# Kernel tuning notes

Hardware: AMD Instinct MI355X
Metric: run time of the kernel (lower is better)

Reference implementation:

```python
import jax, jax.numpy as jnp
import numpy as np

N = 50000          # nodes
E = 800000         # edges
H, C = 8, 32       # heads, channels per head
HC = H * C         # 256
IN = 4             # input feature dim
SLOPE = 0.2        # LeakyReLU negative slope (PyG default)
EPS = 1e-16        # PyG softmax denominator eps


def gat_layer(x, src, dst, ea, W, a_s, a_d, W_e, a_e, b, add_self_loops):
    """Single PyG-style GATConv with edge_dim=1. x:[N,in], ea:[E,1]."""
    if add_self_loops:
        # fill_value='mean': self-loop edge_attr = mean of incoming edge_attr per node
        ones = jnp.ones((src.shape[0], 1), ea.dtype)
        cnt = jax.ops.segment_sum(ones, dst, num_segments=N)
        loop_ea = jax.ops.segment_sum(ea, dst, num_segments=N) / jnp.maximum(cnt, 1.0)
        loop = jnp.arange(N, dtype=src.dtype)
        src = jnp.concatenate([src, loop])
        dst = jnp.concatenate([dst, loop])
        ea = jnp.concatenate([ea, loop_ea], axis=0)
    h = (x @ W).reshape(-1, H, C)                       # [N,H,C] shared src/dst proj
    al_s = jnp.einsum('nhc,hc->nh', h, a_s)              # [N,H]
    al_d = jnp.einsum('nhc,hc->nh', h, a_d)              # [N,H]
    # lin_edge is [1 -> H*C] with no bias, so (lin_edge(ea) * att_edge).sum(-1)
    # collapses to ea * w_e with w_e[h] = sum_c W_e[h,c]*a_e[h,c]
    w_e = jnp.sum(W_e * a_e, axis=-1)                    # [H]
    logits = al_s[src] + al_d[dst] + ea * w_e[None, :]   # [E,H]
    logits = jax.nn.leaky_relu(logits, SLOPE)
    # segment softmax over destination node
    m = jax.ops.segment_max(logits, dst, num_segments=N)
    m = jnp.where(jnp.isfinite(m), m, 0.0)
    p = jnp.exp(logits - m[dst])
    denom = jax.ops.segment_sum(p, dst, num_segments=N)
    alpha = p / (denom[dst] + EPS)                       # [E,H]
    out = jax.ops.segment_sum(h[src] * alpha[:, :, None], dst, num_segments=N)
    return out.reshape(-1, HC) + b                       # concat heads + bias


def setup_inputs() -> dict:
    key = jax.random.key(0)
    ks = jax.random.split(key, 24)
    inp = {
        'x': jax.random.normal(ks[0], (N, IN), jnp.float32),
        'edge_index': jax.random.randint(ks[1], (2, E), 0, N, jnp.int32),
        'edge_attr': jax.random.uniform(ks[2], (E, 1), jnp.float32),
    }
    in_dims = [IN, HC, HC]
    ki = 3
    for l in range(3):
        d = in_dims[l]
        inp[f'W{l+1}'] = jax.random.normal(ks[ki], (d, HC), jnp.float32) * (1.0 / np.sqrt(d)); ki += 1
        inp[f'as{l+1}'] = jax.random.normal(ks[ki], (H, C), jnp.float32) * 0.1; ki += 1
        inp[f'ad{l+1}'] = jax.random.normal(ks[ki], (H, C), jnp.float32) * 0.1; ki += 1
        inp[f'We{l+1}'] = jax.random.normal(ks[ki], (H, C), jnp.float32) * 0.1; ki += 1
        inp[f'ae{l+1}'] = jax.random.normal(ks[ki], (H, C), jnp.float32) * 0.1; ki += 1
        inp[f'b{l+1}'] = jnp.zeros((HC,), jnp.float32)
    return inp


def reference(x, edge_index, edge_attr,
              W1, as1, ad1, We1, ae1, b1,
              W2, as2, ad2, We2, ae2, b2,
              W3, as3, ad3, We3, ae3, b3):
    src, dst = edge_index[0], edge_index[1]
    h = jax.nn.relu(gat_layer(x, src, dst, edge_attr, W1, as1, ad1, We1, ae1, b1, False))
    h = jax.nn.relu(gat_layer(h, src, dst, edge_attr, W2, as2, ad2, We2, ae2, b2, True))
    h = jax.nn.relu(gat_layer(h, src, dst, edge_attr, W3, as3, ad3, We3, ae3, b3, True))
    return h
```

## Files before the change

### kernel.cpp

```cpp
#include <hip/hip_runtime.h>
#include <hip/hip_fp16.h>
#include <math.h>

#define HEADS 8
#define HC 256
#define SLOPE 0.2f
#define SM_EPS 1e-16f
#define LDA 40

typedef __attribute__((ext_vector_type(4))) _Float16 half4v;
typedef __attribute__((ext_vector_type(8))) _Float16 half8;
typedef __attribute__((ext_vector_type(4))) float f32x4;

__global__ void hist_kernel(const int* __restrict__ dst, int* __restrict__ cnt,
                            int* __restrict__ rank, int E) {
  int e = blockIdx.x * blockDim.x + threadIdx.x;
  if (e < E) rank[e] = atomicAdd(&cnt[dst[e]], 1);
}

__global__ void scan_blocks(const int* __restrict__ cnt, int* __restrict__ excl,
                            int* __restrict__ bsums, int N) {
  __shared__ int wsum[16];
  int t = threadIdx.x;
  int i = blockIdx.x * 1024 + t;
  int v = (i < N) ? cnt[i] : 0;
  int lane = t & 63, w = t >> 6;
  int s = v;
  #pragma unroll
  for (int off = 1; off < 64; off <<= 1) {
    int u = __shfl_up(s, off);
    if (lane >= off) s += u;
  }
  if (lane == 63) wsum[w] = s;
  __syncthreads();
  if (w == 0) {
    int ws = (lane < 16) ? wsum[lane] : 0;
    #pragma unroll
    for (int off = 1; off < 16; off <<= 1) {
      int u = __shfl_up(ws, off);
      if (lane >= off) ws += u;
    }
    if (lane < 16) wsum[lane] = ws;
  }
  __syncthreads();
  int wo = (w == 0) ? 0 : wsum[w - 1];
  int incl = s + wo;
  if (i < N) excl[i] = incl - v;
  if (t == 1023) bsums[blockIdx.x] = incl;
}

__global__ void scan_sums(int* __restrict__ bsums, int nb) {
  int lane = threadIdx.x;
  int carry = 0;
  for (int c0 = 0; c0 < nb; c0 += 64) {
    int idx = c0 + lane;
    int v = (idx < nb) ? bsums[idx] : 0;
    int s = v;
    #pragma unroll
    for (int off = 1; off < 64; off <<= 1) {
      int u = __shfl_up(s, off);
      if (lane >= off) s += u;
    }
    if (idx < nb) bsums[idx] = carry + s - v;
    carry += __shfl(s, 63);
  }
}

__global__ void scan_apply(const int* __restrict__ bsums, int* __restrict__ row_ptr,
                           int N, int E) {
  int i = blockIdx.x * blockDim.x + threadIdx.x;
  if (i < N) row_ptr[i] += bsums[i >> 10];
  if (i == 0) row_ptr[N] = E;
}

__global__ void fill_kernel(const int* __restrict__ src, const int* __restrict__ dst,
                            const float* __restrict__ ea, const int* __restrict__ row_ptr,
                            const int* __restrict__ rank, int2* __restrict__ srcea, int E) {
  int e = blockIdx.x * blockDim.x + threadIdx.x;
  if (e < E) {
    int pos = row_ptr[dst[e]] + rank[e];
    srcea[pos] = make_int2(src[e], __float_as_int(ea[e]));
  }
}

__global__ void prep_kernel(const float* __restrict__ W2, __half* __restrict__ WT2,
                            const float* __restrict__ W3, __half* __restrict__ WT3,
                            const float* __restrict__ We1, const float* __restrict__ ae1,
                            const float* __restrict__ We2, const float* __restrict__ ae2,
                            const float* __restrict__ We3, const float* __restrict__ ae3,
                            float* __restrict__ wev,
                            const float* __restrict__ W1, const float* __restrict__ as1,
                            const float* __restrict__ ad1, float* __restrict__ vsd) {
  int b = blockIdx.x;
  int t = threadIdx.x;
  if (b < 256) {
    WT2[t * HC + b] = (__half)W2[b * HC + t];
  } else if (b < 512) {
    int k = b - 256;
    WT3[t * HC + k] = (__half)W3[k * HC + t];
  } else if (b < 515) {
    if (t >= 64) return;
    int l = b - 512;
    const float* We = (l == 0) ? We1 : (l == 1) ? We2 : We3;
    const float* ae = (l == 0) ? ae1 : (l == 1) ? ae2 : ae3;
    float p = 0.f;
    #pragma unroll
    for (int i = 0; i < 4; i++) p += We[t * 4 + i] * ae[t * 4 + i];
    p += __shfl_xor(p, 1);
    p += __shfl_xor(p, 2);
    p += __shfl_xor(p, 4);
    if ((t & 7) == 0) wev[l * 8 + (t >> 3)] = p;
  } else {
    if (t >= 64) return;
    int which = t >> 5;
    int idx = t & 31;
    int h = idx >> 2, k = idx & 3;
    const float* a = which ? ad1 : as1;
    float p = 0.f;
    #pragma unroll
    for (int c = 0; c < 32; c++) p += W1[k * HC + h * 32 + c] * a[h * 32 + c];
    vsd[which * 32 + idx] = p;
  }
}

__global__ __launch_bounds__(256) void mfma_gemm(
    const __half* __restrict__ A, const __half* __restrict__ WT,
    const float* __restrict__ a_s, const float* __restrict__ a_d,
    __half* __restrict__ Hh, float* __restrict__ als, float* __restrict__ ald, int M) {
  __shared__ _Float16 sA[64 * LDA], sB[128 * LDA];
  int t = threadIdx.x;
  int bm = blockIdx.x >> 1, bn = blockIdx.x & 1;
  int m0 = bm * 64, n0 = bn * 128;
  int wave = t >> 6, lane = t & 63, quad = lane >> 4, l16 = lane & 15;
  int sr = t >> 2;
  int sk = (t & 3) * 8;

  f32x4 acc[8];
  #pragma unroll
  for (int c = 0; c < 8; c++) acc[c] = (f32x4){0.f, 0.f, 0.f, 0.f};

  size_t ar = (size_t)min(m0 + sr, M - 1) * HC;
  size_t br0 = (size_t)(n0 + sr) * HC;
  size_t br1 = (size_t)(n0 + sr + 64) * HC;

  half8 pA = *(const half8*)(A + ar + sk);
  half8 pB0 = *(const half8*)(WT + br0 + sk);
  half8 pB1 = *(const half8*)(WT + br1 + sk);

  for (int k0 = 0; k0 < HC; k0 += 32) {
    __syncthreads();
    *(half8*)(sA + sr * LDA + sk) = pA;
    *(half8*)(sB + sr * LDA + sk) = pB0;
    *(half8*)(sB + (sr + 64) * LDA + sk) = pB1;
    __syncthreads();
    int kn = k0 + 32;
    if (kn < HC) {
      pA = *(const half8*)(A + ar + kn + sk);
      pB0 = *(const half8*)(WT + br0 + kn + sk);
      pB1 = *(const half8*)(WT + br1 + kn + sk);
    }
    half8 av = *(const half8*)(sA + (wave * 16 + l16) * LDA + quad * 8);
    #pragma unroll
    for (int c = 0; c < 8; c++) {
      half8 bv = *(const half8*)(sB + (c * 16 + l16) * LDA + quad * 8);
      acc[c] = __builtin_amdgcn_mfma_f32_16x16x32_f16(av, bv, acc[c], 0, 0, 0);
    }
  }

  float asv[8], adv[8];
  #pragma unroll
  for (int c = 0; c < 8; c++) {
    int col = n0 + c * 16 + l16;
    asv[c] = a_s[col];
    adv[c] = a_d[col];
  }
  #pragma unroll
  for (int reg = 0; reg < 4; reg++) {
    int m = m0 + wave * 16 + quad * 4 + reg;
    bool ok = (m < M);
    if (ok) {
      #pragma unroll
      for (int c = 0; c < 8; c++)
        Hh[(size_t)m * HC + n0 + c * 16 + l16] = (__half)acc[c][reg];
    }
    #pragma unroll
    for (int d = 0; d < 4; d++) {
      float ps = acc[2 * d][reg] * asv[2 * d] + acc[2 * d + 1][reg] * asv[2 * d + 1];
      float pd = acc[2 * d][reg] * adv[2 * d] + acc[2 * d + 1][reg] * adv[2 * d + 1];
      #pragma unroll
      for (int mm = 1; mm < 16; mm <<= 1) {
        ps += __shfl_xor(ps, mm);
        pd += __shfl_xor(pd, mm);
      }
      if (ok && l16 == 0) {
        als[(size_t)m * HEADS + (n0 >> 5) + d] = ps;
        ald[(size_t)m * HEADS + (n0 >> 5) + d] = pd;
      }
    }
  }
}

__global__ __launch_bounds__(256) void accum_l1_kernel(
    const int2* __restrict__ srcea, const int* __restrict__ row_ptr,
    const float* __restrict__ x, const float* __restrict__ W,
    const float* __restrict__ vsd, const float* __restrict__ wev,
    const float* __restrict__ bias, __half* __restrict__ Ah, int N) {
  int n = blockIdx.x * 4 + (threadIdx.x >> 6);
  if (n >= N) return;
  int lane = threadIdx.x & 63;
  int h_t = lane >> 3;
  int cbase = lane * 4;
  int base = row_ptr[n], deg = row_ptr[n + 1] - base;
  int ubase = __builtin_amdgcn_readfirstlane(base);
  int udeg = __builtin_amdgcn_readfirstlane(deg);
  float we_h = wev[h_t];
  float4 vs4 = *(const float4*)(vsd + h_t * 4);
  float4 vd4 = *(const float4*)(vsd + 32 + h_t * 4);
  float4 wr0 = *(const float4*)(W + 0 * HC + cbase);
  float4 wr1 = *(const float4*)(W + 1 * HC + cbase);
  float4 wr2 = *(const float4*)(W + 2 * HC + cbase);
  float4 wr3 = *(const float4*)(W + 3 * HC + cbase);
  float4 xn = *(const float4*)(x + (size_t)n * 4);
  float ald_h = xn.x * vd4.x + xn.y * vd4.y + xn.z * vd4.z + xn.w * vd4.w;

  float den = 0.f;
  float4 acc = make_float4(0.f, 0.f, 0.f, 0.f);
  #pragma unroll 8
  for (int j = 0; j < udeg; j++) {
    int2 se = srcea[ubase + j];
    int s = se.x;
    float eav = __int_as_float(se.y);
    float4 xv = *(const float4*)(x + (size_t)s * 4);
    float l = xv.x * vs4.x + xv.y * vs4.y + xv.z * vs4.z + xv.w * vs4.w
              + ald_h + eav * we_h;
    l = (l > 0.f) ? l : SLOPE * l;
    float p = __expf(l);
    den += p;
    float h0 = xv.x * wr0.x + xv.y * wr1.x + xv.z * wr2.x + xv.w * wr3.x;
    float h1 = xv.x * wr0.y + xv.y * wr1.y + xv.z * wr2.y + xv.w * wr3.y;
    float h2 = xv.x * wr0.z + xv.y * wr1.z + xv.z * wr2.z + xv.w * wr3.z;
    float h3 = xv.x * wr0.w + xv.y * wr1.w + xv.z * wr2.w + xv.w * wr3.w;
    acc.x = fmaf(p, h0, acc.x);
    acc.y = fmaf(p, h1, acc.y);
    acc.z = fmaf(p, h2, acc.z);
    acc.w = fmaf(p, h3, acc.w);
  }

  float rinv = 1.0f / (den + SM_EPS);
  float4 o;
  o.x = fmaxf(fmaf(acc.x, rinv, bias[cbase + 0]), 0.f);
  o.y = fmaxf(fmaf(acc.y, rinv, bias[cbase + 1]), 0.f);
  o.z = fmaxf(fmaf(acc.z, rinv, bias[cbase + 2]), 0.f);
  o.w = fmaxf(fmaf(acc.w, rinv, bias[cbase + 3]), 0.f);
  half4v hv;
  hv.x = (_Float16)o.x;
  hv.y = (_Float16)o.y;
  hv.z = (_Float16)o.z;
  hv.w = (_Float16)o.w;
  *(half4v*)(Ah + (size_t)n * HC + cbase) = hv;
}

template <int SPLIT>
__global__ __launch_bounds__(256) void accum_kernel(
    const int2* __restrict__ srcea, const int* __restrict__ row_ptr,
    const __half* __restrict__ h, const float* __restrict__ als,
    const float* __restrict__ ald, const float* __restrict__ wev,
    const float* __restrict__ bias, float* __restrict__ out,
    __half* __restrict__ Ah, int N) {
  int n = blockIdx.x * 4 + (threadIdx.x >> 6);
  if (n >= N) return;
  int lane = threadIdx.x & 63;
  int h_t = lane >> 3;
  int base = row_ptr[n], deg = row_ptr[n + 1] - base;
  int ubase = __builtin_amdgcn_readfirstlane(base);
  int udeg = __builtin_amdgcn_readfirstlane(deg);
  float ald_h = ald[(size_t)n * HEADS + h_t];
  float we_h = wev[h_t];

  float den = 0.f, easum = 0.f;
  float4 acc = make_float4(0.f, 0.f, 0.f, 0.f);
  #pragma unroll 8
  for (int j = 0; j < udeg; j++) {
    int2 se = srcea[ubase + j];
    int s = se.x;
    float eav = __int_as_float(se.y);
    easum += eav;
    float l = als[(size_t)s * HEADS + h_t] + ald_h + eav * we_h;
    l = (l > 0.f) ? l : SLOPE * l;
    float p = __expf(l);
    den += p;
    const half4v hv = *(const half4v*)(h + (size_t)s * HC + lane * 4);
    acc.x = fmaf(p, (float)hv.x, acc.x);
    acc.y = fmaf(p, (float)hv.y, acc.y);
    acc.z = fmaf(p, (float)hv.z, acc.z);
    acc.w = fmaf(p, (float)hv.w, acc.w);
  }
  {
    float mean_ea = easum / fmaxf((float)udeg, 1.0f);
    float l = als[(size_t)n * HEADS + h_t] + ald_h + mean_ea * we_h;
    l = (l > 0.f) ? l : SLOPE * l;
    float p = __expf(l);
    den += p;
    const half4v hv = *(const half4v*)(h + (size_t)n * HC + lane * 4);
    acc.x = fmaf(p, (float)hv.x, acc.x);
    acc.y = fmaf(p, (float)hv.y, acc.y);
    acc.z = fmaf(p, (float)hv.z, acc.z);
    acc.w = fmaf(p, (float)hv.w, acc.w);
  }

  float rinv = 1.0f / (den + SM_EPS);
  int cbase = lane * 4;
  float4 o;
  o.x = fmaxf(fmaf(acc.x, rinv, bias[cbase + 0]), 0.f);
  o.y = fmaxf(fmaf(acc.y, rinv, bias[cbase + 1]), 0.f);
  o.z = fmaxf(fmaf(acc.z, rinv, bias[cbase + 2]), 0.f);
  o.w = fmaxf(fmaf(acc.w, rinv, bias[cbase + 3]), 0.f);
  if (SPLIT) {
    half4v hv;
    hv.x = (_Float16)o.x;
    hv.y = (_Float16)o.y;
    hv.z = (_Float16)o.z;
    hv.w = (_Float16)o.w;
    *(half4v*)(Ah + (size_t)n * HC + cbase) = hv;
  } else {
    *(float4*)(out + (size_t)n * HC + cbase) = o;
  }
}

extern "C" void kernel_launch(void* const* d_in, const int* in_sizes, int n_in,
                              void* d_out, int out_size, void* d_ws, size_t ws_size,
                              hipStream_t stream) {
  const float* x = (const float*)d_in[0];
  const int* ei = (const int*)d_in[1];
  const float* ea = (const float*)d_in[2];
  int N = in_sizes[0] / 4;
  int E = in_sizes[1] / 2;
  const int* src = ei;
  const int* dst = ei + E;

  const float* W[3];
  const float* Asw[3];
  const float* Adw[3];
  const float* Wew[3];
  const float* Aew[3];
  const float* Bw[3];
  for (int l = 0; l < 3; l++) {
    W[l]   = (const float*)d_in[3 + 6 * l + 0];
    Asw[l] = (const float*)d_in[3 + 6 * l + 1];
    Adw[l] = (const float*)d_in[3 + 6 * l + 2];
    Wew[l] = (const float*)d_in[3 + 6 * l + 3];
    Aew[l] = (const float*)d_in[3 + 6 * l + 4];
    Bw[l]  = (const float*)d_in[3 + 6 * l + 5];
  }

  char* w = (char*)d_ws;
  auto alloc = [&](size_t bytes) {
    char* p = w;
    w += (bytes + 255) & ~(size_t)255;
    return p;
  };
  __half* Hh    = (__half*)alloc((size_t)N * HC * 2);
  __half* Ah    = (__half*)alloc((size_t)N * HC * 2);
  int2* srcea   = (int2*)alloc((size_t)E * 8);
  int* rank     = (int*)alloc((size_t)E * 4);
  __half* WT2   = (__half*)alloc((size_t)HC * HC * 2);
  __half* WT3   = (__half*)alloc((size_t)HC * HC * 2);
  float* als    = (float*)alloc((size_t)N * HEADS * 4);
  float* ald    = (float*)alloc((size_t)N * HEADS * 4);
  float* wev    = (float*)alloc(24 * 4);
  float* vsd    = (float*)alloc(64 * 4);
  int* cnt      = (int*)alloc((size_t)N * 4);
  int* row_ptr  = (int*)alloc(((size_t)N + 1) * 4);
  int* bsums    = (int*)alloc(((size_t)N / 1024 + 2) * 4);
  float* outf = (float*)d_out;

  int nb = (N + 1023) / 1024;
  (void)hipMemsetAsync(cnt, 0, (size_t)N * 4, stream);
  hist_kernel<<<(E + 255) / 256, 256, 0, stream>>>(dst, cnt, rank, E);
  scan_blocks<<<nb, 1024, 0, stream>>>(cnt, row_ptr, bsums, N);
  scan_sums<<<1, 64, 0, stream>>>(bsums, nb);
  scan_apply<<<(N + 255) / 256, 256, 0, stream>>>(bsums, row_ptr, N, E);
  fill_kernel<<<(E + 255) / 256, 256, 0, stream>>>(src, dst, ea, row_ptr, rank,
                                                   srcea, E);
  prep_kernel<<<516, 256, 0, stream>>>(W[1], WT2, W[2], WT3,
                                       Wew[0], Aew[0], Wew[1], Aew[1],
                                       Wew[2], Aew[2], wev,
                                       W[0], Asw[0], Adw[0], vsd);

  int agg_grid = (N + 3) / 4;
  int gemm_grid = ((N + 63) / 64) * 2;

  accum_l1_kernel<<<agg_grid, 256, 0, stream>>>(srcea, row_ptr, x, W[0], vsd,
                                                wev + 0, Bw[0], Ah, N);

  mfma_gemm<<<gemm_grid, 256, 0, stream>>>(Ah, WT2, Asw[1], Adw[1], Hh, als, ald, N);
  accum_kernel<1><<<agg_grid, 256, 0, stream>>>(srcea, row_ptr, Hh, als, ald,
                                                wev + 8, Bw[1], nullptr, Ah, N);

  mfma_gemm<<<gemm_grid, 256, 0, stream>>>(Ah, WT3, Asw[2], Adw[2], Hh, als, ald, N);
  accum_kernel<0><<<agg_grid, 256, 0, stream>>>(srcea, row_ptr, Hh, als, ald,
                                                wev + 16, Bw[2], outf, nullptr, N);
}
```

Measured before the change: 403.6 us.

## Process two nodes per wavefront in aggregation and fuse block-sum scan

The aggregation kernel now has each wavefront handle two destination nodes and interleave their edge loops, so more independent gathers are in flight per wave. This hides gather latency at the cost of more registers and a tail loop for the degree mismatch. Separately, the scan's block-sum pass moves into scan_blocks using a last-block-done atomic counter, which removes one kernel launch. The last-block scan handles at most 64 blocks, which covers N=50000.

```diff
diff --git a/kernel.cpp b/kernel.cpp
--- a/kernel.cpp
+++ b/kernel.cpp
@@ -19,8 +19,10 @@
 }
 
 __global__ void scan_blocks(const int* __restrict__ cnt, int* __restrict__ excl,
-                            int* __restrict__ bsums, int N) {
+                            int* __restrict__ bsums, int* __restrict__ done,
+                            int N, int nb) {
   __shared__ int wsum[16];
+  __shared__ int amlast;
   int t = threadIdx.x;
   int i = blockIdx.x * 1024 + t;
   int v = (i < N) ? cnt[i] : 0;
@@ -46,23 +48,26 @@
   int wo = (w == 0) ? 0 : wsum[w - 1];
   int incl = s + wo;
   if (i < N) excl[i] = incl - v;
-  if (t == 1023) bsums[blockIdx.x] = incl;
-}
-
-__global__ void scan_sums(int* __restrict__ bsums, int nb) {
-  int lane = threadIdx.x;
-  int carry = 0;
-  for (int c0 = 0; c0 < nb; c0 += 64) {
-    int idx = c0 + lane;
-    int v = (idx < nb) ? bsums[idx] : 0;
-    int s = v;
-    #pragma unroll
-    for (int off = 1; off < 64; off <<= 1) {
-      int u = __shfl_up(s, off);
-      if (lane >= off) s += u;
-    }
-    if (idx < nb) bsums[idx] = carry + s - v;
-    carry += __shfl(s, 63);
+  if (t == 1023) {
+    bsums[blockIdx.x] = incl;
+    __threadfence();
+    int old = atomicAdd(done, 1);
+    amlast = (old == nb - 1) ? 1 : 0;
+  }
+  __syncthreads();
+  if (amlast) {
+    __threadfence();
+    if (t < 64) {
+      int idx = t;
+      int bv = (idx < nb) ? bsums[idx] : 0;
+      int bs = bv;
+      #pragma unroll
+      for (int off = 1; off < 64; off <<= 1) {
+        int u = __shfl_up(bs, off);
+        if (t >= off) bs += u;
+      }
+      if (idx < nb) bsums[idx] = bs - bv;
+    }
   }
 }
 
@@ -267,63 +272,144 @@
     const float* __restrict__ ald, const float* __restrict__ wev,
     const float* __restrict__ bias, float* __restrict__ out,
     __half* __restrict__ Ah, int N) {
-  int n = blockIdx.x * 4 + (threadIdx.x >> 6);
-  if (n >= N) return;
+  int n0 = blockIdx.x * 8 + (threadIdx.x >> 6) * 2;
+  if (n0 >= N) return;
+  int n1 = n0 + 1;
+  bool has1 = (n1 < N);
   int lane = threadIdx.x & 63;
   int h_t = lane >> 3;
-  int base = row_ptr[n], deg = row_ptr[n + 1] - base;
-  int ubase = __builtin_amdgcn_readfirstlane(base);
-  int udeg = __builtin_amdgcn_readfirstlane(deg);
-  float ald_h = ald[(size_t)n * HEADS + h_t];
+  int cbase = lane * 4;
+
+  int base0 = row_ptr[n0], deg0 = row_ptr[n0 + 1] - base0;
+  int ub0 = __builtin_amdgcn_readfirstlane(base0);
+  int ud0 = __builtin_amdgcn_readfirstlane(deg0);
+  int ub1 = 0, ud1 = 0;
+  if (has1) {
+    int base1 = row_ptr[n1], deg1 = row_ptr[n1 + 1] - base1;
+    ub1 = __builtin_amdgcn_readfirstlane(base1);
+    ud1 = __builtin_amdgcn_readfirstlane(deg1);
+  }
   float we_h = wev[h_t];
-
-  float den = 0.f, easum = 0.f;
-  float4 acc = make_float4(0.f, 0.f, 0.f, 0.f);
-  #pragma unroll 8
-  for (int j = 0; j < udeg; j++) {
-    int2 se = srcea[ubase + j];
-    int s = se.x;
-    float eav = __int_as_float(se.y);
-    easum += eav;
-    float l = als[(size_t)s * HEADS + h_t] + ald_h + eav * we_h;
+  float ald0 = ald[(size_t)n0 * HEADS + h_t];
+  float ald1 = has1 ? ald[(size_t)n1 * HEADS + h_t] : 0.f;
+
+  float den0 = 0.f, ea0 = 0.f, den1 = 0.f, ea1 = 0.f;
+  float4 acc0 = make_float4(0.f, 0.f, 0.f, 0.f);
+  float4 acc1 = make_float4(0.f, 0.f, 0.f, 0.f);
+
+  int mind = min(ud0, ud1);
+  #pragma unroll 4
+  for (int j = 0; j < mind; j++) {
+    int2 sa = srcea[ub0 + j];
+    int2 sb = srcea[ub1 + j];
+    float eava = __int_as_float(sa.y);
+    float eavb = __int_as_float(sb.y);
+    ea0 += eava;
+    ea1 += eavb;
+    float la = als[(size_t)sa.x * HEADS + h_t] + ald0 + eava * we_h;
+    float lb = als[(size_t)sb.x * HEADS + h_t] + ald1 + eavb * we_h;
+    la = (la > 0.f) ? la : SLOPE * la;
+    lb = (lb > 0.f) ? lb : SLOPE * lb;
+    float pa = __expf(la);
+    float pb = __expf(lb);
+    den0 += pa;
+    den1 += pb;
+    const half4v ha = *(const half4v*)(h + (size_t)sa.x * HC + cbase);
+    const half4v hb = *(const half4v*)(h + (size_t)sb.x * HC + cbase);
+    acc0.x = fmaf(pa, (float)ha.x, acc0.x);
+    acc0.y = fmaf(pa, (float)ha.y, acc0.y);
+    acc0.z = fmaf(pa, (float)ha.z, acc0.z);
+    acc0.w = fmaf(pa, (float)ha.w, acc0.w);
+    acc1.x = fmaf(pb, (float)hb.x, acc1.x);
+    acc1.y = fmaf(pb, (float)hb.y, acc1.y);
+    acc1.z = fmaf(pb, (float)hb.z, acc1.z);
+    acc1.w = fmaf(pb, (float)hb.w, acc1.w);
+  }
+  #pragma unroll 4
+  for (int j = mind; j < ud0; j++) {
+    int2 sa = srcea[ub0 + j];
+    float eava = __int_as_float(sa.y);
+    ea0 += eava;
+    float la = als[(size_t)sa.x * HEADS + h_t] + ald0 + eava * we_h;
+    la = (la > 0.f) ? la : SLOPE * la;
+    float pa = __expf(la);
+    den0 += pa;
+    const half4v ha = *(const half4v*)(h + (size_t)sa.x * HC + cbase);
+    acc0.x = fmaf(pa, (float)ha.x, acc0.x);
+    acc0.y = fmaf(pa, (float)ha.y, acc0.y);
+    acc0.z = fmaf(pa, (float)ha.z, acc0.z);
+    acc0.w = fmaf(pa, (float)ha.w, acc0.w);
+  }
+  #pragma unroll 4
+  for (int j = mind; j < ud1; j++) {
+    int2 sb = srcea[ub1 + j];
+    float eavb = __int_as_float(sb.y);
+    ea1 += eavb;
+    float lb = als[(size_t)sb.x * HEADS + h_t] + ald1 + eavb * we_h;
+    lb = (lb > 0.f) ? lb : SLOPE * lb;
+    float pb = __expf(lb);
+    den1 += pb;
+    const half4v hb = *(const half4v*)(h + (size_t)sb.x * HC + cbase);
+    acc1.x = fmaf(pb, (float)hb.x, acc1.x);
+    acc1.y = fmaf(pb, (float)hb.y, acc1.y);
+    acc1.z = fmaf(pb, (float)hb.z, acc1.z);
+    acc1.w = fmaf(pb, (float)hb.w, acc1.w);
+  }
+
+  float b0 = bias[cbase + 0], b1 = bias[cbase + 1];
+  float b2 = bias[cbase + 2], b3 = bias[cbase + 3];
+
+  {
+    float mean_ea = ea0 / fmaxf((float)ud0, 1.0f);
+    float l = als[(size_t)n0 * HEADS + h_t] + ald0 + mean_ea * we_h;
     l = (l > 0.f) ? l : SLOPE * l;
     float p = __expf(l);
-    den += p;
-    const half4v hv = *(const half4v*)(h + (size_t)s * HC + lane * 4);
-    acc.x = fmaf(p, (float)hv.x, acc.x);
-    acc.y = fmaf(p, (float)hv.y, acc.y);
-    acc.z = fmaf(p, (float)hv.z, acc.z);
-    acc.w = fmaf(p, (float)hv.w, acc.w);
-  }
-  {
-    float mean_ea = easum / fmaxf((float)udeg, 1.0f);
-    float l = als[(size_t)n * HEADS + h_t] + ald_h + mean_ea * we_h;
+    den0 += p;
+    const half4v hv = *(const half4v*)(h + (size_t)n0 * HC + cbase);
+    acc0.x = fmaf(p, (float)hv.x, acc0.x);
+    acc0.y = fmaf(p, (float)hv.y, acc0.y);
+    acc0.z = fmaf(p, (float)hv.z, acc0.z);
+    acc0.w = fmaf(p, (float)hv.w, acc0.w);
+    float rinv = 1.0f / (den0 + SM_EPS);
+    float4 o;
+    o.x = fmaxf(fmaf(acc0.x, rinv, b0), 0.f);
+    o.y = fmaxf(fmaf(acc0.y, rinv, b1), 0.f);
+    o.z = fmaxf(fmaf(acc0.z, rinv, b2), 0.f);
+    o.w = fmaxf(fmaf(acc0.w, rinv, b3), 0.f);
+    if (SPLIT) {
+      half4v hw;
+      hw.x = (_Float16)o.x; hw.y = (_Float16)o.y;
+      hw.z = (_Float16)o.z; hw.w = (_Float16)o.w;
+      *(half4v*)(Ah + (size_t)n0 * HC + cbase) = hw;
+    } else {
+      *(float4*)(out + (size_t)n0 * HC + cbase) = o;
+    }
+  }
+  if (has1) {
+    float mean_ea = ea1 / fmaxf((float)ud1, 1.0f);
+    float l = als[(size_t)n1 * HEADS + h_t] + ald1 + mean_ea * we_h;
     l = (l > 0.f) ? l : SLOPE * l;
     float p = __expf(l);
-    den += p;
-    const half4v hv = *(const half4v*)(h + (size_t)n * HC + lane * 4);
-    acc.x = fmaf(p, (float)hv.x, acc.x);
-    acc.y = fmaf(p, (float)hv.y, acc.y);
-    acc.z = fmaf(p, (float)hv.z, acc.z);
-    acc.w = fmaf(p, (float)hv.w, acc.w);
-  }
-
-  float rinv = 1.0f / (den + SM_EPS);
-  int cbase = lane * 4;
-  float4 o;
-  o.x = fmaxf(fmaf(acc.x, rinv, bias[cbase + 0]), 0.f);
-  o.y = fmaxf(fmaf(acc.y, rinv, bias[cbase + 1]), 0.f);
-  o.z = fmaxf(fmaf(acc.z, rinv, bias[cbase + 2]), 0.f);
-  o.w = fmaxf(fmaf(acc.w, rinv, bias[cbase + 3]), 0.f);
-  if (SPLIT) {
-    half4v hv;
-    hv.x = (_Float16)o.x;
-    hv.y = (_Float16)o.y;
-    hv.z = (_Float16)o.z;
-    hv.w = (_Float16)o.w;
-    *(half4v*)(Ah + (size_t)n * HC + cbase) = hv;
-  } else {
-    *(float4*)(out + (size_t)n * HC + cbase) = o;
+    den1 += p;
+    const half4v hv = *(const half4v*)(h + (size_t)n1 * HC + cbase);
+    acc1.x = fmaf(p, (float)hv.x, acc1.x);
+    acc1.y = fmaf(p, (float)hv.y, acc1.y);
+    acc1.z = fmaf(p, (float)hv.z, acc1.z);
+    acc1.w = fmaf(p, (float)hv.w, acc1.w);
+    float rinv = 1.0f / (den1 + SM_EPS);
+    float4 o;
+    o.x = fmaxf(fmaf(acc1.x, rinv, b0), 0.f);
+    o.y = fmaxf(fmaf(acc1.y, rinv, b1), 0.f);
+    o.z = fmaxf(fmaf(acc1.z, rinv, b2), 0.f);
+    o.w = fmaxf(fmaf(acc1.w, rinv, b3), 0.f);
+    if (SPLIT) {
+      half4v hw;
+      hw.x = (_Float16)o.x; hw.y = (_Float16)o.y;
+      hw.z = (_Float16)o.z; hw.w = (_Float16)o.w;
+      *(half4v*)(Ah + (size_t)n1 * HC + cbase) = hw;
+    } else {
+      *(float4*)(out + (size_t)n1 * HC + cbase) = o;
+    }
   }
 }
 
@@ -369,16 +455,15 @@
   float* ald    = (float*)alloc((size_t)N * HEADS * 4);
   float* wev    = (float*)alloc(24 * 4);
   float* vsd    = (float*)alloc(64 * 4);
-  int* cnt      = (int*)alloc((size_t)N * 4);
+  int* cnt      = (int*)alloc(((size_t)N + 1) * 4);
   int* row_ptr  = (int*)alloc(((size_t)N + 1) * 4);
   int* bsums    = (int*)alloc(((size_t)N / 1024 + 2) * 4);
   float* outf = (float*)d_out;
 
   int nb = (N + 1023) / 1024;
-  (void)hipMemsetAsync(cnt, 0, (size_t)N * 4, stream);
+  (void)hipMemsetAsync(cnt, 0, ((size_t)N + 1) * 4, stream);
   hist_kernel<<<(E + 255) / 256, 256, 0, stream>>>(dst, cnt, rank, E);
-  scan_blocks<<<nb, 1024, 0, stream>>>(cnt, row_ptr, bsums, N);
-  scan_sums<<<1, 64, 0, stream>>>(bsums, nb);
+  scan_blocks<<<nb, 1024, 0, stream>>>(cnt, row_ptr, bsums, cnt + N, N, nb);
   scan_apply<<<(N + 255) / 256, 256, 0, stream>>>(bsums, row_ptr, N, E);
   fill_kernel<<<(E + 255) / 256, 256, 0, stream>>>(src, dst, ea, row_ptr, rank,
                                                    srcea, E);
@@ -388,16 +473,17 @@
                                        W[0], Asw[0], Adw[0], vsd);
 
   int agg_grid = (N + 3) / 4;
+  int agg2_grid = (N + 7) / 8;
   int gemm_grid = ((N + 63) / 64) * 2;
 
   accum_l1_kernel<<<agg_grid, 256, 0, stream>>>(srcea, row_ptr, x, W[0], vsd,
                                                 wev + 0, Bw[0], Ah, N);
 
   mfma_gemm<<<gemm_grid, 256, 0, stream>>>(Ah, WT2, Asw[1], Adw[1], Hh, als, ald, N);
-  accum_kernel<1><<<agg_grid, 256, 0, stream>>>(srcea, row_ptr, Hh, als, ald,
-                                                wev + 8, Bw[1], nullptr, Ah, N);
+  accum_kernel<1><<<agg2_grid, 256, 0, stream>>>(srcea, row_ptr, Hh, als, ald,
+                                                 wev + 8, Bw[1], nullptr, Ah, N);
 
   mfma_gemm<<<gemm_grid, 256, 0, stream>>>(Ah, WT3, Asw[2], Adw[2], Hh, als, ald, N);
-  accum_kernel<0><<<agg_grid, 256, 0, stream>>>(srcea, row_ptr, Hh, als, ald,
-                                                wev + 16, Bw[2], outf, nullptr, N);
-}
+  accum_kernel<0><<<agg2_grid, 256, 0, stream>>>(srcea, row_ptr, Hh, als, ald,
+                                                 wev + 16, Bw[2], outf, nullptr, N);
+}
```

New measurement: 419.6 us. 3.9% more time.
